# Kernel optimization log

Measured on AMD Instinct MI355X. Metric: run time of the kernel, lower is better.

## Reference

```python
import jax, jax.numpy as jnp
import numpy as np

B, N, D, H = 128, 2048, 512, 512

def setup_inputs() -> dict:
    key = jax.random.key(0)
    ks = jax.random.split(key, 8)
    x = jax.random.normal(ks[0], (B, D), dtype=jnp.float32)
    context = jax.random.normal(ks[1], (B, N, D), dtype=jnp.float32)
    mask = jax.random.randint(ks[2], (B, 1, N), 0, 2) > 0  # True = masked out
    Wi = jax.random.normal(ks[3], (H, D), dtype=jnp.float32) * 0.02
    bi = jnp.zeros((H,), dtype=jnp.float32)
    Wc = jax.random.normal(ks[4], (H, D), dtype=jnp.float32) * 0.02
    bc = jnp.zeros((H,), dtype=jnp.float32)
    V = jax.random.uniform(ks[5], (H,), dtype=jnp.float32, minval=-1.0, maxval=1.0)
    return {"x": x, "context": context, "mask": mask,
            "Wi": Wi, "bi": bi, "Wc": Wc, "bc": bc, "V": V}

def reference(x, context, mask, Wi, bi, Wc, bc, V):
    # input_linear: [B, H]
    inp = x @ Wi.T + bi
    # context_linear (Conv1d kernel=1 == pointwise linear): [B, N, H]
    ctx = jnp.einsum('bnd,hd->bnh', context, Wc) + bc
    # additive (Bahdanau) score: V . tanh(inp + ctx) -> [B, N]
    att = jnp.einsum('h,bnh->bn', V, jnp.tanh(inp[:, None, :] + ctx))
    att = jnp.where(mask[:, 0, :], -jnp.inf, att)
    alpha = jax.nn.softmax(att, axis=-1)
    log_p = jax.nn.log_softmax(att, axis=-1)
    # context mixing: bmm(ctx^T [B,H,N], alpha [B,N,1]) -> [B, H]
    hidden_state = jnp.einsum('bnh,bn->bh', ctx, alpha)
    return hidden_state, alpha, log_p
```

## Files before the change

### kernel.cpp

```cpp
#include <hip/hip_runtime.h>
#include <hip/hip_bf16.h>
#include <math.h>

#define B_ 128
#define N_ 2048
#define D_ 512
#define H_ 512

#define NEG_BIG (-1.0e30f)

typedef unsigned int uint;
typedef unsigned short ushort;

#define WS_INP  0
#define WS_ATT  (WS_INP + B_*H_)
#define WS_M    (WS_ATT + B_*N_)
#define WS_FLAG (WS_M + B_*D_)
#define WS_BP   393280
#define WS_NEED_FLOATS (WS_BP + 262144)

typedef __attribute__((ext_vector_type(4))) float  f32x4;
typedef __attribute__((ext_vector_type(8))) short  bf16x8;

union BF8 { unsigned short u[8]; bf16x8 v; };

__device__ __forceinline__ ushort f2bf(float x) {
    uint u = __float_as_uint(x);
    u = (u + 0x7fffu + ((u >> 16) & 1u)) >> 16;
    return (ushort)u;
}
__device__ __forceinline__ float bf2f(ushort h) {
    return __uint_as_float(((uint)h) << 16);
}
__device__ __forceinline__ float fast_tanh(float x) {
    return 1.0f - 2.0f / (1.0f + __expf(2.0f * x));
}

__global__ __launch_bounds__(256) void prep_kernel(
        const float* __restrict__ Wc, ushort* __restrict__ Bp,
        const float* __restrict__ x, const float* __restrict__ Wi,
        const float* __restrict__ bi, float* __restrict__ inp,
        const uint* __restrict__ mask_raw, int* __restrict__ flag) {
    const int bid = blockIdx.x;
    const int t   = threadIdx.x;

    if (bid < 128) {
        int tid = bid * 256 + t;
        int lane = tid & 63;
        int fs   = tid >> 6;
        int hf = fs >> 4, ks = fs & 15;
        int h  = hf * 16 + (lane & 15);
        int k0 = ks * 32 + (lane >> 4) * 8;
        const float* src = Wc + (size_t)h * D_ + k0;
        BF8 hi, lo;
#pragma unroll
        for (int j = 0; j < 8; ++j) {
            float xv = src[j];
            hi.u[j] = f2bf(xv);
            lo.u[j] = f2bf(xv - bf2f(hi.u[j]));
        }
        *(bf16x8*)(Bp + (size_t)tid * 8)          = hi.v;
        *(bf16x8*)(Bp + 262144 + (size_t)tid * 8) = lo.v;
    } else if (bid < 384) {
        int idx = (bid - 128) * 256 + t;
        int b = idx >> 9;
        int h = idx & (H_ - 1);
        const float4* ar = (const float4*)(x + (size_t)b * D_);
        const float4* wr = (const float4*)(Wi + (size_t)h * D_);
        float acc = 0.f;
#pragma unroll 4
        for (int d = 0; d < D_ / 4; ++d) {
            float4 av = ar[d], wv = wr[d];
            acc = fmaf(av.x, wv.x, acc);
            acc = fmaf(av.y, wv.y, acc);
            acc = fmaf(av.z, wv.z, acc);
            acc = fmaf(av.w, wv.w, acc);
        }
        inp[idx] = acc + bi[h];
    } else if (t < 64) {
        uint v = mask_raw[t];
        unsigned long long m = __ballot(v <= 1u);
        if (t == 0) *flag = (m == ~0ull) ? 1 : 0;
    }
}

__global__ __launch_bounds__(256) void linear_kernel(
        const float* __restrict__ a, const float* __restrict__ W,
        const float* __restrict__ bias, float* __restrict__ out) {
    int idx = blockIdx.x * 256 + threadIdx.x;
    int b = idx >> 9;
    int h = idx & (H_ - 1);
    const float4* ar = (const float4*)(a + (size_t)b * D_);
    const float4* wr = (const float4*)(W + (size_t)h * D_);
    float acc = 0.f;
#pragma unroll 4
    for (int d = 0; d < D_ / 4; ++d) {
        float4 av = ar[d], wv = wr[d];
        acc = fmaf(av.x, wv.x, acc);
        acc = fmaf(av.y, wv.y, acc);
        acc = fmaf(av.z, wv.z, acc);
        acc = fmaf(av.w, wv.w, acc);
    }
    out[idx] = acc + bias[h];
}

#define KP  32
#define NPH 16

#define DMA_B(p, bi) do {                                                       \
    _Pragma("unroll")                                                           \
    for (int i_ = 0; i_ < 4; ++i_) {                                            \
        int c_  = w * 4 + i_;                                                   \
        int hf_ = c_ & 31;                                                      \
        const ushort* g_ = Bp + (c_ >= 32 ? 262144 : 0)                         \
                         + (size_t)((hf_ << 4) + (p)) * 512 + lane * 8;         \
        ushort* l_ = (c_ >= 32 ? sBl[bi] : sBh[bi]) + hf_ * 512;                \
        __builtin_amdgcn_global_load_lds(                                       \
            (const __attribute__((address_space(1))) unsigned int*)g_,          \
            (__attribute__((address_space(3))) unsigned int*)l_, 16, 0, 0);     \
    }                                                                           \
} while (0)

#define STAGE_A2(Ux, Wx, bi) do {                                               \
    uint h0_ = (Ux.y & 0xFFFF0000u) | (Ux.x >> 16);                             \
    uint h1_ = (Ux.w & 0xFFFF0000u) | (Ux.z >> 16);                             \
    uint h2_ = (Wx.y & 0xFFFF0000u) | (Wx.x >> 16);                             \
    uint h3_ = (Wx.w & 0xFFFF0000u) | (Wx.z >> 16);                             \
    float r0_ = __uint_as_float(Ux.x) - __uint_as_float(Ux.x & 0xFFFF0000u);    \
    float r1_ = __uint_as_float(Ux.y) - __uint_as_float(Ux.y & 0xFFFF0000u);    \
    float r2_ = __uint_as_float(Ux.z) - __uint_as_float(Ux.z & 0xFFFF0000u);    \
    float r3_ = __uint_as_float(Ux.w) - __uint_as_float(Ux.w & 0xFFFF0000u);    \
    float r4_ = __uint_as_float(Wx.x) - __uint_as_float(Wx.x & 0xFFFF0000u);    \
    float r5_ = __uint_as_float(Wx.y) - __uint_as_float(Wx.y & 0xFFFF0000u);    \
    float r6_ = __uint_as_float(Wx.z) - __uint_as_float(Wx.z & 0xFFFF0000u);    \
    float r7_ = __uint_as_float(Wx.w) - __uint_as_float(Wx.w & 0xFFFF0000u);    \
    uint l0_ = (__float_as_uint(r1_) & 0xFFFF0000u) | (__float_as_uint(r0_) >> 16); \
    uint l1_ = (__float_as_uint(r3_) & 0xFFFF0000u) | (__float_as_uint(r2_) >> 16); \
    uint l2_ = (__float_as_uint(r5_) & 0xFFFF0000u) | (__float_as_uint(r4_) >> 16); \
    uint l3_ = (__float_as_uint(r7_) & 0xFFFF0000u) | (__float_as_uint(r6_) >> 16); \
    *(uint4*)((char*)sAh[bi] + aw) = make_uint4(h0_, h1_, h2_, h3_);            \
    *(uint4*)((char*)sAl[bi] + aw) = make_uint4(l0_, l1_, l2_, l3_);            \
} while (0)

#define MM(a_, b_, c_) __builtin_amdgcn_mfma_f32_16x16x32_bf16(a_, b_, c_, 0, 0, 0)

__global__ __launch_bounds__(1024, 4) void att_mfma_kernel(
        const float* __restrict__ ctx, const ushort* __restrict__ Bp,
        const float* __restrict__ bc, const float* __restrict__ V,
        const float* __restrict__ inp, float* __restrict__ att) {
    __shared__ ushort sAh[2][4096];
    __shared__ ushort sAl[2][4096];
    __shared__ ushort sBh[2][16384];
    __shared__ ushort sBl[2][16384];

    const int t    = threadIdx.x;
    const int lane = t & 63;
    const int w    = t >> 6;
    const int wr   = w >> 2;
    const int wc   = w & 3;
    const int g0   = blockIdx.x * 128;
    const int b    = g0 >> 11;

    const int srow = t >> 2;
    const int skc  = t & 3;
    const float* gAs = ctx + (size_t)(g0 + srow) * D_ + skc * 8;
    unsigned aw = ((unsigned)(srow >> 4) << 10) | ((unsigned)skc << 8)
                | ((unsigned)(srow & 15) << 4);
    aw ^= ((aw >> 8) & 3u) << 4;
    const bool stager = (t < 512);

    unsigned ar0 = ((unsigned)(wr * 2 + 0) << 10) | ((unsigned)lane << 4);
    ar0 ^= ((ar0 >> 8) & 3u) << 4;
    unsigned ar1 = ((unsigned)(wr * 2 + 1) << 10) | ((unsigned)lane << 4);
    ar1 ^= ((ar1 >> 8) & 3u) << 4;

    f32x4 acc[2][8] = {};

    {
        uint4 U0, W0;
        if (stager) {
            U0 = *(const uint4*)(gAs);
            W0 = *(const uint4*)(gAs + 4);
        }
        DMA_B(0, 0);
        if (stager) STAGE_A2(U0, W0, 0);
        __syncthreads();
    }

    for (int p = 0; p < NPH; ++p) {
        const int buf = p & 1;
        const int pn  = (p + 1) & 15;

        bf16x8 ah0 = *(const bf16x8*)((const char*)sAh[buf] + ar0);
        bf16x8 al0 = *(const bf16x8*)((const char*)sAl[buf] + ar0);
        bf16x8 ah1 = *(const bf16x8*)((const char*)sAh[buf] + ar1);
        bf16x8 al1 = *(const bf16x8*)((const char*)sAl[buf] + ar1);

        uint4 U, Wv;
        if (stager) {
            U  = *(const uint4*)(gAs + pn * KP);
            Wv = *(const uint4*)(gAs + pn * KP + 4);
        }
        DMA_B(pn, buf ^ 1);

        __builtin_amdgcn_s_setprio(1);
#pragma unroll
        for (int cf = 0; cf < 8; ++cf) {
            const int bo = (wc * 8 + cf) * 512 + lane * 8;
            bf16x8 bh = *(const bf16x8*)&sBh[buf][bo];
            bf16x8 bl = *(const bf16x8*)&sBl[buf][bo];
            acc[0][cf] = MM(ah0, bh, acc[0][cf]);
            acc[1][cf] = MM(ah1, bh, acc[1][cf]);
            acc[0][cf] = MM(ah0, bl, acc[0][cf]);
            acc[1][cf] = MM(ah1, bl, acc[1][cf]);
            acc[0][cf] = MM(al0, bh, acc[0][cf]);
            acc[1][cf] = MM(al1, bh, acc[1][cf]);
        }
        __builtin_amdgcn_s_setprio(0);

        if (stager) STAGE_A2(U, Wv, buf ^ 1);
        __syncthreads();
    }

    float P[2][4] = {};
#pragma unroll
    for (int cf = 0; cf < 8; ++cf) {
        const int h = wc * 128 + cf * 16 + (lane & 15);
        const float sh = inp[b * H_ + h] + bc[h];
        const float vh = V[h];
#pragma unroll
        for (int rf = 0; rf < 2; ++rf)
#pragma unroll
            for (int j = 0; j < 4; ++j)
                P[rf][j] += vh * fast_tanh(acc[rf][cf][j] + sh);
    }
#pragma unroll
    for (int rf = 0; rf < 2; ++rf)
#pragma unroll
        for (int j = 0; j < 4; ++j) {
            float x = P[rf][j];
            x += __shfl_xor(x, 1); x += __shfl_xor(x, 2);
            x += __shfl_xor(x, 4); x += __shfl_xor(x, 8);
            P[rf][j] = x;
        }

    float (*red)[32] = (float(*)[32])sAh;
    if ((lane & 15) == 0) {
        const int kc = lane >> 4;
#pragma unroll
        for (int rf = 0; rf < 2; ++rf)
#pragma unroll
            for (int j = 0; j < 4; ++j)
                red[w][rf * 16 + kc * 4 + j] = P[rf][j];
    }
    __syncthreads();
    if (t < 128) {
        const int wr2 = t >> 5, r = t & 31;
        att[g0 + wr2 * 32 + r] = red[wr2 * 4 + 0][r] + red[wr2 * 4 + 1][r]
                               + red[wr2 * 4 + 2][r] + red[wr2 * 4 + 3][r];
    }
}

__global__ __launch_bounds__(256) void softmax_kernel(
        const float* __restrict__ att, const void* __restrict__ mask,
        const int* __restrict__ flag, float* __restrict__ alpha,
        float* __restrict__ logp) {
    __shared__ float row[N_];
    __shared__ float red[4];
    const int b = blockIdx.x, t = threadIdx.x;
    const int is_int = *flag;
    const int* mi = (const int*)mask;
    const unsigned char* mb = (const unsigned char*)mask;

    float lmax = -INFINITY;
    for (int n = t; n < N_; n += 256) {
        bool m = is_int ? (mi[b * N_ + n] != 0) : (mb[b * N_ + n] != 0);
        float a = m ? NEG_BIG : att[b * N_ + n];
        row[n] = a;
        lmax = fmaxf(lmax, a);
    }
#pragma unroll
    for (int off = 32; off; off >>= 1) lmax = fmaxf(lmax, __shfl_down(lmax, off));
    if ((t & 63) == 0) red[t >> 6] = lmax;
    __syncthreads();
    const float rmax = fmaxf(fmaxf(red[0], red[1]), fmaxf(red[2], red[3]));
    __syncthreads();

    float lsum = 0.f;
    for (int n = t; n < N_; n += 256) lsum += __expf(row[n] - rmax);
#pragma unroll
    for (int off = 32; off; off >>= 1) lsum += __shfl_down(lsum, off);
    if ((t & 63) == 0) red[t >> 6] = lsum;
    __syncthreads();
    const float s = red[0] + red[1] + red[2] + red[3];
    const float inv = 1.0f / s;
    const float lse = logf(s);

    for (int n = t; n < N_; n += 256) {
        float a = row[n];
        alpha[b * N_ + n] = __expf(a - rmax) * inv;
        logp[b * N_ + n]  = a - rmax - lse;
    }
}

__global__ __launch_bounds__(512) void wsum_kernel(
        const float* __restrict__ context, const float* __restrict__ alpha,
        float* __restrict__ m) {
    __shared__ float al[N_];
    __shared__ float part[3][128];
    const int c = blockIdx.x;
    const int b = blockIdx.y;
    const int t = threadIdx.x;
    for (int n = t; n < N_; n += 512) al[n] = alpha[(size_t)b * N_ + n];
    __syncthreads();
    const int d = c * 128 + (t & 127);
    const int q = t >> 7;
    const float* cp = context + (size_t)b * N_ * D_ + (size_t)q * 512 * D_ + d;
    const float* ap = al + q * 512;
    float acc = 0.f;
#pragma unroll 8
    for (int n = 0; n < 512; ++n) acc = fmaf(ap[n], cp[(size_t)n * D_], acc);
    if (q) part[q - 1][t & 127] = acc;
    __syncthreads();
    if (q == 0)
        m[b * D_ + d] = acc + part[0][t & 127] + part[1][t & 127] + part[2][t & 127];
}

extern "C" void kernel_launch(void* const* d_in, const int* in_sizes, int n_in,
                              void* d_out, int out_size, void* d_ws, size_t ws_size,
                              hipStream_t stream) {
    const float* x       = (const float*)d_in[0];
    const float* context = (const float*)d_in[1];
    const void*  mask    = d_in[2];
    const float* Wi      = (const float*)d_in[3];
    const float* bi      = (const float*)d_in[4];
    const float* Wc      = (const float*)d_in[5];
    const float* bc      = (const float*)d_in[6];
    const float* V       = (const float*)d_in[7];

    float* out  = (float*)d_out;
    float* ws   = (float*)d_ws;
    float* inp  = ws + WS_INP;
    float* att  = ws + WS_ATT;
    float* m    = ws + WS_M;
    int*   flag = (int*)(ws + WS_FLAG);

    float* hidden = out;
    float* alpha  = out + B_ * H_;
    float* logp   = alpha + B_ * N_;

    ushort* Bp =
        (ws_size >= (size_t)WS_NEED_FLOATS * 4) ? (ushort*)(ws + WS_BP)
                                                : (ushort*)logp;

    prep_kernel<<<385, 256, 0, stream>>>(Wc, Bp, x, Wi, bi, inp,
                                         (const uint*)mask, flag);
    att_mfma_kernel<<<(B_ * N_) / 128, 1024, 0, stream>>>(context, Bp, bc, V, inp, att);
    softmax_kernel<<<B_, 256, 0, stream>>>(att, mask, flag, alpha, logp);
    wsum_kernel<<<dim3(4, B_), 512, 0, stream>>>(context, alpha, m);
    linear_kernel<<<256, 256, 0, stream>>>(m, Wc, bc, hidden);
}
```

Baseline: 527.6 us.

## Switch attention GEMM from 16x16x32 to 32x32x16 bf16 MFMA tiles

Replaces the 16x16x32 bf16 MFMA tiling with 32x32x16 MFMA. The prepacked Wc fragment layout, the LDS A-tile layout and its swizzle, and the epilogue reduction all change to match the 32x32 accumulator layout. The larger tile cuts the number of MFMA issues and B-fragment LDS reads per unit of work. In exchange the epilogue needs more shuffle-reduction steps, and the new swizzle could add LDS bank conflicts.

New measurement: 576.7 us. +9.3%, slower.

```diff
diff --git a/kernel.cpp b/kernel.cpp
--- a/kernel.cpp
+++ b/kernel.cpp
@@ -19,8 +19,9 @@
 #define WS_BP   393280
 #define WS_NEED_FLOATS (WS_BP + 262144)
 
-typedef __attribute__((ext_vector_type(4))) float  f32x4;
-typedef __attribute__((ext_vector_type(8))) short  bf16x8;
+typedef __attribute__((ext_vector_type(4)))  float  f32x4;
+typedef __attribute__((ext_vector_type(16))) float  f32x16;
+typedef __attribute__((ext_vector_type(8)))  short  bf16x8;
 
 union BF8 { unsigned short u[8]; bf16x8 v; };
 
@@ -47,10 +48,10 @@
     if (bid < 128) {
         int tid = bid * 256 + t;
         int lane = tid & 63;
-        int fs   = tid >> 6;
-        int hf = fs >> 4, ks = fs & 15;
-        int h  = hf * 16 + (lane & 15);
-        int k0 = ks * 32 + (lane >> 4) * 8;
+        int frag = tid >> 6;
+        int cg = frag >> 5, kf = frag & 31;
+        int h  = cg * 32 + (lane & 31);
+        int k0 = kf * 16 + (lane >> 5) * 8;
         const float* src = Wc + (size_t)h * D_ + k0;
         BF8 hi, lo;
 #pragma unroll
@@ -110,11 +111,12 @@
 #define DMA_B(p, bi) do {                                                       \
     _Pragma("unroll")                                                           \
     for (int i_ = 0; i_ < 4; ++i_) {                                            \
-        int c_  = w * 4 + i_;                                                   \
-        int hf_ = c_ & 31;                                                      \
+        int c_  = w * 4 + i_;                                        \
+        int c6_ = c_ & 31;                                        \
         const ushort* g_ = Bp + (c_ >= 32 ? 262144 : 0)                         \
-                         + (size_t)((hf_ << 4) + (p)) * 512 + lane * 8;         \
-        ushort* l_ = (c_ >= 32 ? sBl[bi] : sBh[bi]) + hf_ * 512;                \
+                         + (size_t)((c6_ >> 1) * 32 + (p) * 2 + (c6_ & 1)) * 512 \
+                         + lane * 8;                                            \
+        ushort* l_ = (c_ >= 32 ? sBl[bi] : sBh[bi]) + c6_ * 512;                \
         __builtin_amdgcn_global_load_lds(                                       \
             (const __attribute__((address_space(1))) unsigned int*)g_,          \
             (__attribute__((address_space(3))) unsigned int*)l_, 16, 0, 0);     \
@@ -142,7 +144,7 @@
     *(uint4*)((char*)sAl[bi] + aw) = make_uint4(l0_, l1_, l2_, l3_);            \
 } while (0)
 
-#define MM(a_, b_, c_) __builtin_amdgcn_mfma_f32_16x16x32_bf16(a_, b_, c_, 0, 0, 0)
+#define MM32(a_, b_, c_) __builtin_amdgcn_mfma_f32_32x32x16_bf16(a_, b_, c_, 0, 0, 0)
 
 __global__ __launch_bounds__(1024, 4) void att_mfma_kernel(
         const float* __restrict__ ctx, const ushort* __restrict__ Bp,
@@ -164,17 +166,21 @@
     const int srow = t >> 2;
     const int skc  = t & 3;
     const float* gAs = ctx + (size_t)(g0 + srow) * D_ + skc * 8;
-    unsigned aw = ((unsigned)(srow >> 4) << 10) | ((unsigned)skc << 8)
-                | ((unsigned)(srow & 15) << 4);
-    aw ^= ((aw >> 8) & 3u) << 4;
+    const int sfrag = (srow >> 5) * 2 + (skc >> 1);
+    const int slh   = skc & 1;
+    const int sslot = (slh * 32) + ((srow & 31) ^ ((sfrag * 2 + slh) & 7));
+    const unsigned aw = (unsigned)(sfrag * 1024 + sslot * 16);
     const bool stager = (t < 512);
 
-    unsigned ar0 = ((unsigned)(wr * 2 + 0) << 10) | ((unsigned)lane << 4);
-    ar0 ^= ((ar0 >> 8) & 3u) << 4;
-    unsigned ar1 = ((unsigned)(wr * 2 + 1) << 10) | ((unsigned)lane << 4);
-    ar1 ^= ((ar1 >> 8) & 3u) << 4;
-
-    f32x4 acc[2][8] = {};
+    unsigned ard[2];
+#pragma unroll
+    for (int kf = 0; kf < 2; ++kf) {
+        const int frag = wr * 2 + kf;
+        const int s = (frag * 2 + (lane >> 5)) & 7;
+        ard[kf] = (unsigned)(frag * 1024 + (lane ^ s) * 16);
+    }
+
+    f32x16 acc[4] = {};
 
     {
         uint4 U0, W0;
@@ -191,10 +197,12 @@
         const int buf = p & 1;
         const int pn  = (p + 1) & 15;
 
-        bf16x8 ah0 = *(const bf16x8*)((const char*)sAh[buf] + ar0);
-        bf16x8 al0 = *(const bf16x8*)((const char*)sAl[buf] + ar0);
-        bf16x8 ah1 = *(const bf16x8*)((const char*)sAh[buf] + ar1);
-        bf16x8 al1 = *(const bf16x8*)((const char*)sAl[buf] + ar1);
+        bf16x8 ah[2], al[2];
+#pragma unroll
+        for (int kf = 0; kf < 2; ++kf) {
+            ah[kf] = *(const bf16x8*)((const char*)sAh[buf] + ard[kf]);
+            al[kf] = *(const bf16x8*)((const char*)sAl[buf] + ard[kf]);
+        }
 
         uint4 U, Wv;
         if (stager) {
@@ -205,16 +213,17 @@
 
         __builtin_amdgcn_s_setprio(1);
 #pragma unroll
-        for (int cf = 0; cf < 8; ++cf) {
-            const int bo = (wc * 8 + cf) * 512 + lane * 8;
-            bf16x8 bh = *(const bf16x8*)&sBh[buf][bo];
-            bf16x8 bl = *(const bf16x8*)&sBl[buf][bo];
-            acc[0][cf] = MM(ah0, bh, acc[0][cf]);
-            acc[1][cf] = MM(ah1, bh, acc[1][cf]);
-            acc[0][cf] = MM(ah0, bl, acc[0][cf]);
-            acc[1][cf] = MM(ah1, bl, acc[1][cf]);
-            acc[0][cf] = MM(al0, bh, acc[0][cf]);
-            acc[1][cf] = MM(al1, bh, acc[1][cf]);
+        for (int cf = 0; cf < 4; ++cf) {
+            const int cg = wc * 4 + cf;
+#pragma unroll
+            for (int kfl = 0; kfl < 2; ++kfl) {
+                const int bo = (cg * 2 + kfl) * 512 + lane * 8;
+                bf16x8 bh = *(const bf16x8*)&sBh[buf][bo];
+                bf16x8 bl = *(const bf16x8*)&sBl[buf][bo];
+                acc[cf] = MM32(ah[kfl], bh, acc[cf]);
+                acc[cf] = MM32(ah[kfl], bl, acc[cf]);
+                acc[cf] = MM32(al[kfl], bh, acc[cf]);
+            }
         }
         __builtin_amdgcn_s_setprio(0);
 
@@ -222,36 +231,35 @@
         __syncthreads();
     }
 
-    float P[2][4] = {};
-#pragma unroll
-    for (int cf = 0; cf < 8; ++cf) {
-        const int h = wc * 128 + cf * 16 + (lane & 15);
+    float p16[16];
+#pragma unroll
+    for (int r = 0; r < 16; ++r) p16[r] = 0.f;
+#pragma unroll
+    for (int cf = 0; cf < 4; ++cf) {
+        const int h = wc * 128 + cf * 32 + (lane & 31);
         const float sh = inp[b * H_ + h] + bc[h];
         const float vh = V[h];
 #pragma unroll
-        for (int rf = 0; rf < 2; ++rf)
-#pragma unroll
-            for (int j = 0; j < 4; ++j)
-                P[rf][j] += vh * fast_tanh(acc[rf][cf][j] + sh);
-    }
-#pragma unroll
-    for (int rf = 0; rf < 2; ++rf)
-#pragma unroll
-        for (int j = 0; j < 4; ++j) {
-            float x = P[rf][j];
-            x += __shfl_xor(x, 1); x += __shfl_xor(x, 2);
-            x += __shfl_xor(x, 4); x += __shfl_xor(x, 8);
-            P[rf][j] = x;
-        }
+        for (int r = 0; r < 16; ++r)
+            p16[r] += vh * fast_tanh(acc[cf][r] + sh);
+    }
+#pragma unroll
+    for (int r = 0; r < 16; ++r) {
+        float x = p16[r];
+        x += __shfl_xor(x, 1); x += __shfl_xor(x, 2);
+        x += __shfl_xor(x, 4); x += __shfl_xor(x, 8);
+        x += __shfl_xor(x, 16);
+        p16[r] = x;
+    }
 
     float (*red)[32] = (float(*)[32])sAh;
-    if ((lane & 15) == 0) {
-        const int kc = lane >> 4;
-#pragma unroll
-        for (int rf = 0; rf < 2; ++rf)
-#pragma unroll
-            for (int j = 0; j < 4; ++j)
-                red[w][rf * 16 + kc * 4 + j] = P[rf][j];
+    if ((lane & 31) == 0) {
+        const int lh = lane >> 5;
+#pragma unroll
+        for (int r = 0; r < 16; ++r) {
+            const int row = (r & 3) + 8 * (r >> 2) + 4 * lh;
+            red[w][row] = p16[r];
+        }
     }
     __syncthreads();
     if (t < 128) {
```
